# Performance work log

Hardware: AMD Instinct MI355X
Metric: run time of the kernel (lower is better)

The kernel has to match this reference:

```python
import jax, jax.numpy as jnp
import numpy as np

ORD = 2  # matches EarthMoverLoss(ord=2)


def _lsa_square(cost):
    """Optimal linear sum assignment (minimize) on a square cost matrix.
    Shortest-augmenting-path algorithm, equivalent to
    scipy.optimize.linear_sum_assignment. Returns col4row: row i -> col4row[i].
    """
    n = cost.shape[0]
    u = np.zeros(n)
    v = np.zeros(n)
    path = np.full(n, -1, dtype=np.int64)
    col4row = np.full(n, -1, dtype=np.int64)
    row4col = np.full(n, -1, dtype=np.int64)
    rows = np.arange(n)
    for cur_row in range(n):
        min_val = 0.0
        i = cur_row
        SR = np.zeros(n, dtype=bool)   # scanned rows
        SC = np.zeros(n, dtype=bool)   # scanned cols
        shortest = np.full(n, np.inf)  # shortest path cost to each col
        sink = -1
        while sink == -1:
            SR[i] = True
            cols = np.flatnonzero(~SC)
            r = min_val + cost[i, cols] - u[i] - v[cols]
            upd = r < shortest[cols]
            cu = cols[upd]
            shortest[cu] = r[upd]
            path[cu] = i
            k = np.argmin(shortest[cols])
            j = cols[k]
            min_val = shortest[j]
            if np.isinf(min_val):
                raise ValueError('infeasible cost matrix')
            SC[j] = True
            if row4col[j] == -1:
                sink = j
            else:
                i = row4col[j]
        # dual variable update
        u[cur_row] += min_val
        others = SR & (rows != cur_row)
        u[others] += min_val - shortest[col4row[others]]
        v[SC] -= min_val - shortest[SC]
        # augment along the alternating path
        j = sink
        while True:
            i = path[j]
            row4col[j] = i
            col4row[i], j = j, col4row[i]
            if i == cur_row:
                break
    return col4row


def _batched_assignment(x, y):
    """Per-sample Euclidean cdist + Hungarian; mirrors the torch module's
    detached CPU/scipy path. Returns [B, N] int permutation of y per sample."""
    xn = np.asarray(jax.device_get(x), dtype=np.float64)
    yn = np.asarray(jax.device_get(y), dtype=np.float64)
    perms = []
    for b in range(xn.shape[0]):
        d2 = ((xn[b, :, None, :] - yn[b, None, :, :]) ** 2).sum(-1)  # [N, N]
        perms.append(_lsa_square(np.sqrt(d2)))
    return jnp.asarray(np.stack(perms))  # [B, N]


def setup_inputs() -> dict:
    key = jax.random.key(0)
    k1, k2 = jax.random.split(key)
    pred = jax.random.normal(k1, (8, 256, 3), dtype=jnp.float32)
    label = jax.random.normal(k2, (8, 256, 3), dtype=jnp.float32)
    return {"pred": pred, "label": label}


def reference(pred, label):
    # Hungarian matching on detached values (scipy returns ind1 = arange for
    # a square cost matrix, so only label is permuted).
    perm = _batched_assignment(pred, label)                      # [B, N]
    matched_y = jnp.take_along_axis(label, perm[:, :, None], axis=1)  # [B, N, D]
    # mean over batch and points of the ord-2 vector norm along coord dim
    return jnp.mean(jnp.linalg.norm(pred - matched_y, ord=ORD, axis=2))
```

## Files before the change

kernel.cpp:

```cpp
#include <hip/hip_runtime.h>
#include <math.h>

#define NPTS 256
#define NB 8

#if __has_builtin(__builtin_amdgcn_sqrtf)
#define FSQRT __builtin_amdgcn_sqrtf
#else
#define FSQRT sqrtf
#endif

__device__ __forceinline__ double dist3d(double ax, double ay, double az,
                                         double bx, double by, double bz) {
#pragma clang fp contract(off)
  double d0 = ax - bx;
  double d1 = ay - by;
  double d2 = az - bz;
  double s = d0 * d0;
  s = s + d1 * d1;
  s = s + d2 * d2;
  return sqrt(s);
}

__device__ __forceinline__ float distf(float ax, float ay, float az,
                                       float bx, float by, float bz) {
  float d0 = ax - bx, d1 = ay - by, d2 = az - bz;
  return FSQRT(d0 * d0 + d1 * d1 + d2 * d2);
}

__device__ __forceinline__ unsigned wave_min_u32(unsigned x) {
  unsigned r = x;
  r = min(r, (unsigned)__builtin_amdgcn_update_dpp((int)r, (int)r, 0x111, 0xF, 0xF, false));
  r = min(r, (unsigned)__builtin_amdgcn_update_dpp((int)r, (int)r, 0x112, 0xF, 0xF, false));
  r = min(r, (unsigned)__builtin_amdgcn_update_dpp((int)r, (int)r, 0x114, 0xF, 0xF, false));
  r = min(r, (unsigned)__builtin_amdgcn_update_dpp((int)r, (int)r, 0x118, 0xF, 0xF, false));
  r = min(r, (unsigned)__builtin_amdgcn_update_dpp((int)r, (int)r, 0x142, 0xF, 0xF, false));
  r = min(r, (unsigned)__builtin_amdgcn_update_dpp((int)r, (int)r, 0x143, 0xF, 0xF, false));
  return (unsigned)__builtin_amdgcn_readlane((int)r, 63);
}

__global__ __launch_bounds__(64) void emd_lsa_kernel(
    const float* __restrict__ pred, const float* __restrict__ label,
    double* __restrict__ partial) {
  __shared__ float4 rowd[NPTS];
  __shared__ float4 colj[NPTS];
  __shared__ float short_l[NPTS];
  __shared__ int path_l[NPTS];
  __shared__ int c4r_l[NPTS];
  __shared__ int r4c_l[NPTS];
  __shared__ int sr_l[NPTS];
  __shared__ int bcfr[NPTS];
  __shared__ int fq[NPTS];

  const int lane = threadIdx.x;
  const int b = blockIdx.x;
  const float* xg = pred + (size_t)b * NPTS * 3;
  const float* yg = label + (size_t)b * NPTS * 3;

  const int cid0 = lane * 4, cid1 = cid0 + 1, cid2 = cid0 + 2, cid3 = cid0 + 3;

  float q0x, q0y, q0z, q1x, q1y, q1z, q2x, q2y, q2z, q3x, q3y, q3z;
  float vv0, vv1, vv2, vv3;
  int rc0, rc1, rc2, rc3;

#define INITC(c) { int j = cid##c; \
    rowd[j] = make_float4(xg[j*3+0], xg[j*3+1], xg[j*3+2], 0.0f); \
    float t0 = yg[j*3+0], t1 = yg[j*3+1], t2 = yg[j*3+2]; \
    colj[j] = make_float4(t0, t1, t2, 0.0f); \
    q##c##x = t0; q##c##y = t1; q##c##z = t2; \
    c4r_l[j] = -1; r4c_l[j] = -1; bcfr[j] = 0x7FFFFFFF; }
  INITC(0) INITC(1) INITC(2) INITC(3)
#undef INITC
  __syncthreads();

  float mm0 = 3.4e38f, mm1 = 3.4e38f, mm2 = 3.4e38f, mm3 = 3.4e38f;
  int im0 = -1, im1 = -1, im2 = -1, im3 = -1;
  for (int i = 0; i < NPTS; ++i) {
    float4 rd = rowd[i];
#define CRED(c) { float d = distf(rd.x, rd.y, rd.z, q##c##x, q##c##y, q##c##z); \
    bool u_ = d < mm##c; mm##c = u_ ? d : mm##c; im##c = u_ ? i : im##c; }
    CRED(0) CRED(1) CRED(2) CRED(3)
#undef CRED
  }
  colj[cid0].w = mm0; colj[cid1].w = mm1;
  colj[cid2].w = mm2; colj[cid3].w = mm3;
  atomicMin(&bcfr[im0], cid0);
  atomicMin(&bcfr[im1], cid1);
  atomicMin(&bcfr[im2], cid2);
  atomicMin(&bcfr[im3], cid3);
  __syncthreads();
  if (bcfr[im0] == cid0) { r4c_l[cid0] = im0; c4r_l[im0] = cid0; }
  if (bcfr[im1] == cid1) { r4c_l[cid1] = im1; c4r_l[im1] = cid1; }
  if (bcfr[im2] == cid2) { r4c_l[cid2] = im2; c4r_l[im2] = cid2; }
  if (bcfr[im3] == cid3) { r4c_l[cid3] = im3; c4r_l[im3] = cid3; }
  __syncthreads();

  {
    float4 rD0 = rowd[cid0], rD1 = rowd[cid1], rD2 = rowd[cid2], rD3 = rowd[cid3];
    int ja0 = c4r_l[cid0], ja1 = c4r_l[cid1], ja2 = c4r_l[cid2], ja3 = c4r_l[cid3];
    float mu0 = 3.4e38f, mu1 = 3.4e38f, mu2 = 3.4e38f, mu3 = 3.4e38f;
    for (int j = 0; j < NPTS; ++j) {
      float4 cj = colj[j];
#define RT(c) { float d = distf(rD##c.x, rD##c.y, rD##c.z, cj.x, cj.y, cj.z) - cj.w; \
      d = (j == ja##c) ? 3.4e38f : d; \
      mu##c = fminf(mu##c, d); }
      RT(0) RT(1) RT(2) RT(3)
#undef RT
    }
    if (ja0 >= 0) { colj[ja0].w -= mu0; rowd[cid0].w = mu0; }
    if (ja1 >= 0) { colj[ja1].w -= mu1; rowd[cid1].w = mu1; }
    if (ja2 >= 0) { colj[ja2].w -= mu2; rowd[cid2].w = mu2; }
    if (ja3 >= 0) { colj[ja3].w -= mu3; rowd[cid3].w = mu3; }
  }
  __syncthreads();
  vv0 = colj[cid0].w; vv1 = colj[cid1].w;
  vv2 = colj[cid2].w; vv3 = colj[cid3].w;
  rc0 = r4c_l[cid0]; rc1 = r4c_l[cid1]; rc2 = r4c_l[cid2]; rc3 = r4c_l[cid3];

  int nf;
  {
    int4 cc = *(int4*)&c4r_l[cid0];
    bool f0 = cc.x < 0, f1 = cc.y < 0, f2 = cc.z < 0, f3 = cc.w < 0;
    unsigned long long b0 = __ballot(f0), b1 = __ballot(f1);
    unsigned long long b2 = __ballot(f2), b3 = __ballot(f3);
    unsigned long long lt = (1ull << lane) - 1ull;
    int off = __popcll(b0 & lt) + __popcll(b1 & lt) + __popcll(b2 & lt) + __popcll(b3 & lt);
    if (f0) fq[off++] = cid0;
    if (f1) fq[off++] = cid1;
    if (f2) fq[off++] = cid2;
    if (f3) fq[off++] = cid3;
    nf = __popcll(b0) + __popcll(b1) + __popcll(b2) + __popcll(b3);
  }
  __syncthreads();

  const float INF = 3.4e38f;

  for (int t = 0; t < nf; ++t) {
    int cur_row = fq[t];

    float sh0 = INF, sh1 = INF, sh2 = INF, sh3 = INF;
    int pp0 = -1, pp1 = -1, pp2 = -1, pp3 = -1;
    int sc0 = 0, sc1 = 0, sc2 = 0, sc3 = 0;
    *(int4*)&sr_l[cid0] = make_int4(0, 0, 0, 0);

    float4 cr0 = rowd[rc0 < 0 ? 0 : rc0];
    float4 cr1 = rowd[rc1 < 0 ? 0 : rc1];
    float4 cr2 = rowd[rc2 < 0 ? 0 : rc2];
    float4 cr3 = rowd[rc3 < 0 ? 0 : rc3];

    float xi, yi, zi, ui;
    { float4 r0 = rowd[cur_row]; xi = r0.x; yi = r0.y; zi = r0.z; ui = r0.w; }
    __syncthreads();

    float min_val = 0.0f;
    int i = cur_row;
    int sink = -1;

    while (true) {
      sr_l[i] = 1;
      float base = min_val - ui;
      unsigned k0, k1, k2, k3;
#define SSTEP(c) { float d = distf(xi, yi, zi, q##c##x, q##c##y, q##c##z); \
      float r = (base + d) - vv##c; \
      bool u_ = (r < sh##c) && (sc##c == 0); \
      sh##c = u_ ? r : sh##c; \
      pp##c = u_ ? i : pp##c; \
      unsigned kk = (__float_as_uint(fmaxf(sh##c, 0.0f)) & 0xFFFFFF00u) | (unsigned)cid##c; \
      k##c = sc##c ? 0xFFFFFFFFu : kk; }
      SSTEP(0) SSTEP(1) SSTEP(2) SSTEP(3)
#undef SSTEP
      bool t01 = k1 < k0;
      unsigned ka = t01 ? k1 : k0;
      float ea = t01 ? sh1 : sh0; int pa = t01 ? pp1 : pp0; int na = t01 ? rc1 : rc0;
      float axa = t01 ? cr1.x : cr0.x, aya = t01 ? cr1.y : cr0.y;
      float aza = t01 ? cr1.z : cr0.z, aua = t01 ? cr1.w : cr0.w;
      bool t23 = k3 < k2;
      unsigned kb = t23 ? k3 : k2;
      float eb = t23 ? sh3 : sh2; int pb = t23 ? pp3 : pp2; int nb2 = t23 ? rc3 : rc2;
      float axb = t23 ? cr3.x : cr2.x, ayb = t23 ? cr3.y : cr2.y;
      float azb = t23 ? cr3.z : cr2.z, aub = t23 ? cr3.w : cr2.w;
      bool tf = kb < ka;
      unsigned lkey = tf ? kb : ka;
      float el = tf ? eb : ea; int pl = tf ? pb : pa; int nl = tf ? nb2 : na;
      float nx = tf ? axb : axa, ny = tf ? ayb : aya;
      float nz = tf ? azb : aza, nu = tf ? aub : aua;

      unsigned best = wave_min_u32(lkey);
      int jstar = (int)(best & 0xFFu);
      int w = jstar >> 2;

      if (lane == w) {
        short_l[jstar] = el;
        path_l[jstar] = pl;
      }
      sc0 |= (cid0 == jstar); sc1 |= (cid1 == jstar);
      sc2 |= (cid2 == jstar); sc3 |= (cid3 == jstar);

      min_val = __int_as_float(__builtin_amdgcn_readlane(__float_as_int(el), w));
      int nr = __builtin_amdgcn_readlane(nl, w);
      if (nr < 0) { sink = jstar; break; }
      i = nr;
      xi = __int_as_float(__builtin_amdgcn_readlane(__float_as_int(nx), w));
      yi = __int_as_float(__builtin_amdgcn_readlane(__float_as_int(ny), w));
      zi = __int_as_float(__builtin_amdgcn_readlane(__float_as_int(nz), w));
      ui = __int_as_float(__builtin_amdgcn_readlane(__float_as_int(nu), w));
    }
    __syncthreads();

#define DUALU(c) { int row = cid##c; \
      if (sr_l[row]) { \
        float du = (row == cur_row) ? min_val : (min_val - short_l[c4r_l[row]]); \
        rowd[row].w += du; } \
      if (sc##c) vv##c -= min_val - sh##c; }
    DUALU(0) DUALU(1) DUALU(2) DUALU(3)
#undef DUALU
    __syncthreads();

    if (lane == 0) {
      int jj = sink;
      while (true) {
        int ii = path_l[jj];
        r4c_l[jj] = ii;
        int tmp = c4r_l[ii];
        c4r_l[ii] = jj;
        jj = tmp;
        if (ii == cur_row) break;
      }
    }
    __syncthreads();
    rc0 = r4c_l[cid0]; rc1 = r4c_l[cid1]; rc2 = r4c_l[cid2]; rc3 = r4c_l[cid3];
    __syncthreads();
  }

  double s = 0.0;
#define FIN(c) { int row = cid##c; int j = c4r_l[row]; float4 rd = rowd[row]; \
    float4 cj = colj[j]; \
    s += dist3d((double)rd.x, (double)rd.y, (double)rd.z, \
                (double)cj.x, (double)cj.y, (double)cj.z); }
  FIN(0) FIN(1) FIN(2) FIN(3)
#undef FIN
  for (int m = 1; m < 64; m <<= 1) s += __shfl_xor(s, m);
  if (lane == 0) partial[b] = s;
}

__global__ void emd_finalize_kernel(const double* __restrict__ partial,
                                    float* __restrict__ out) {
  if (threadIdx.x == 0 && blockIdx.x == 0) {
    double s = 0.0;
    for (int b = 0; b < NB; ++b) s += partial[b];
    out[0] = (float)(s / (double)(NB * NPTS));
  }
}

extern "C" void kernel_launch(void* const* d_in, const int* in_sizes, int n_in,
                              void* d_out, int out_size, void* d_ws, size_t ws_size,
                              hipStream_t stream) {
  const float* pred = (const float*)d_in[0];
  const float* label = (const float*)d_in[1];
  double* partial = (double*)d_ws;
  emd_lsa_kernel<<<NB, 64, 0, stream>>>(pred, label, partial);
  emd_finalize_kernel<<<1, 64, 0, stream>>>(partial, (float*)d_out);
}
```

Before: 1.278 ms.

## Keep path and assignment arrays in registers, augment via readlane

Drops the shared-memory path, row4col and col4row arrays. Each lane now keeps its own path predecessors and col4row entries in registers, and the augmentation walk runs on the whole wave using readlane instead of serially on lane 0 through LDS. This removes per-step LDS stores of the path, the lane-0 serial augment with its surrounding barriers, and the reload of row4col after every augmentation. In exchange each augment step costs several readlanes and selects across all lanes, and register pressure rises.

```diff
diff --git a/kernel.cpp b/kernel.cpp
--- a/kernel.cpp
+++ b/kernel.cpp
@@ -45,7 +45,6 @@
   __shared__ float4 rowd[NPTS];
   __shared__ float4 colj[NPTS];
   __shared__ float short_l[NPTS];
-  __shared__ int path_l[NPTS];
   __shared__ int c4r_l[NPTS];
   __shared__ int r4c_l[NPTS];
   __shared__ int sr_l[NPTS];
@@ -62,6 +61,7 @@
   float q0x, q0y, q0z, q1x, q1y, q1z, q2x, q2y, q2z, q3x, q3y, q3z;
   float vv0, vv1, vv2, vv3;
   int rc0, rc1, rc2, rc3;
+  int c4rr0, c4rr1, c4rr2, c4rr3;
 
 #define INITC(c) { int j = cid##c; \
     rowd[j] = make_float4(xg[j*3+0], xg[j*3+1], xg[j*3+2], 0.0f); \
@@ -120,6 +120,7 @@
   int nf;
   {
     int4 cc = *(int4*)&c4r_l[cid0];
+    c4rr0 = cc.x; c4rr1 = cc.y; c4rr2 = cc.z; c4rr3 = cc.w;
     bool f0 = cc.x < 0, f1 = cc.y < 0, f2 = cc.z < 0, f3 = cc.w < 0;
     unsigned long long b0 = __ballot(f0), b1 = __ballot(f1);
     unsigned long long b2 = __ballot(f2), b3 = __ballot(f3);
@@ -150,7 +151,6 @@
 
     float xi, yi, zi, ui;
     { float4 r0 = rowd[cur_row]; xi = r0.x; yi = r0.y; zi = r0.z; ui = r0.w; }
-    __syncthreads();
 
     float min_val = 0.0f;
     int i = cur_row;
@@ -171,17 +171,17 @@
 #undef SSTEP
       bool t01 = k1 < k0;
       unsigned ka = t01 ? k1 : k0;
-      float ea = t01 ? sh1 : sh0; int pa = t01 ? pp1 : pp0; int na = t01 ? rc1 : rc0;
+      float ea = t01 ? sh1 : sh0; int na = t01 ? rc1 : rc0;
       float axa = t01 ? cr1.x : cr0.x, aya = t01 ? cr1.y : cr0.y;
       float aza = t01 ? cr1.z : cr0.z, aua = t01 ? cr1.w : cr0.w;
       bool t23 = k3 < k2;
       unsigned kb = t23 ? k3 : k2;
-      float eb = t23 ? sh3 : sh2; int pb = t23 ? pp3 : pp2; int nb2 = t23 ? rc3 : rc2;
+      float eb = t23 ? sh3 : sh2; int nb2 = t23 ? rc3 : rc2;
       float axb = t23 ? cr3.x : cr2.x, ayb = t23 ? cr3.y : cr2.y;
       float azb = t23 ? cr3.z : cr2.z, aub = t23 ? cr3.w : cr2.w;
       bool tf = kb < ka;
       unsigned lkey = tf ? kb : ka;
-      float el = tf ? eb : ea; int pl = tf ? pb : pa; int nl = tf ? nb2 : na;
+      float el = tf ? eb : ea; int nl = tf ? nb2 : na;
       float nx = tf ? axb : axa, ny = tf ? ayb : aya;
       float nz = tf ? azb : aza, nu = tf ? aub : aua;
 
@@ -189,10 +189,7 @@
       int jstar = (int)(best & 0xFFu);
       int w = jstar >> 2;
 
-      if (lane == w) {
-        short_l[jstar] = el;
-        path_l[jstar] = pl;
-      }
+      if (lane == w) short_l[jstar] = el;
       sc0 |= (cid0 == jstar); sc1 |= (cid1 == jstar);
       sc2 |= (cid2 == jstar); sc3 |= (cid3 == jstar);
 
@@ -209,31 +206,44 @@
 
 #define DUALU(c) { int row = cid##c; \
       if (sr_l[row]) { \
-        float du = (row == cur_row) ? min_val : (min_val - short_l[c4r_l[row]]); \
+        float du = (row == cur_row) ? min_val : (min_val - short_l[c4rr##c]); \
         rowd[row].w += du; } \
       if (sc##c) vv##c -= min_val - sh##c; }
     DUALU(0) DUALU(1) DUALU(2) DUALU(3)
 #undef DUALU
-    __syncthreads();
-
-    if (lane == 0) {
+
+    {
       int jj = sink;
       while (true) {
-        int ii = path_l[jj];
-        r4c_l[jj] = ii;
-        int tmp = c4r_l[ii];
-        c4r_l[ii] = jj;
+        int wj = jj >> 2, cj = jj & 3;
+        int plo = (cj & 1) ? pp1 : pp0;
+        int phi = (cj & 1) ? pp3 : pp2;
+        int psel = (cj & 2) ? phi : plo;
+        int ii = __builtin_amdgcn_readlane(psel, wj);
+        bool mej = (lane == wj);
+        rc0 = (mej && cj == 0) ? ii : rc0;
+        rc1 = (mej && cj == 1) ? ii : rc1;
+        rc2 = (mej && cj == 2) ? ii : rc2;
+        rc3 = (mej && cj == 3) ? ii : rc3;
+        int wi = ii >> 2, ci = ii & 3;
+        int clo = (ci & 1) ? c4rr1 : c4rr0;
+        int chi = (ci & 1) ? c4rr3 : c4rr2;
+        int csel = (ci & 2) ? chi : clo;
+        int tmp = __builtin_amdgcn_readlane(csel, wi);
+        bool mei = (lane == wi);
+        c4rr0 = (mei && ci == 0) ? jj : c4rr0;
+        c4rr1 = (mei && ci == 1) ? jj : c4rr1;
+        c4rr2 = (mei && ci == 2) ? jj : c4rr2;
+        c4rr3 = (mei && ci == 3) ? jj : c4rr3;
         jj = tmp;
         if (ii == cur_row) break;
       }
     }
     __syncthreads();
-    rc0 = r4c_l[cid0]; rc1 = r4c_l[cid1]; rc2 = r4c_l[cid2]; rc3 = r4c_l[cid3];
-    __syncthreads();
   }
 
   double s = 0.0;
-#define FIN(c) { int row = cid##c; int j = c4r_l[row]; float4 rd = rowd[row]; \
+#define FIN(c) { int row = cid##c; int j = c4rr##c; float4 rd = rowd[row]; \
     float4 cj = colj[j]; \
     s += dist3d((double)rd.x, (double)rd.y, (double)rd.z, \
                 (double)cj.x, (double)cj.y, (double)cj.z); }
```

After: 1.298 ms. No clear change (+1.6%).
